# Performance work log

Measured on AMD Instinct MI355X. Metric: run time of the kernel, lower is better.

Reference implementation:

```python
import jax, jax.numpy as jnp
import numpy as np

B, D, T, H = 256, 256, 512, 512  # batch, input_dim, seq_len, hidden_dim


def setup_inputs() -> dict:
    key = jax.random.key(0)
    ks = jax.random.split(key, 7)
    s = 1.0 / np.sqrt(H)
    u = lambda k, shape: jax.random.uniform(k, shape, jnp.float32, -s, s)
    return {
        "x": jax.random.normal(ks[0], (B, D, T), jnp.float32),
        "W_ih": u(ks[1], (4 * H, D)),   # gate order: i, f, g, o (PyTorch)
        "W_hh": u(ks[2], (4 * H, H)),
        "b_ih": u(ks[3], (4 * H,)),
        "b_hh": u(ks[4], (4 * H,)),
        "W_mlp": u(ks[5], (1, H)),      # Linear(hidden_dim, num_classes=1)
        "b_mlp": u(ks[6], (1,)),
    }


def reference(x, W_ih, W_hh, b_ih, b_hh, W_mlp, b_mlp):
    # x: (B, D, T) -> (T, B, D), matching the two transposes in LSTM_model
    xs = jnp.transpose(x, (2, 0, 1))
    # Precompute input contributions for all timesteps: (T, B, 4H)
    x_gates = jnp.einsum('tbd,gd->tbg', xs, W_ih) + b_ih + b_hh
    Hh = W_hh.shape[1]

    def step(carry, xg):
        h, c = carry
        g = xg + h @ W_hh.T                      # (B, 4H)
        i = jax.nn.sigmoid(g[:, 0 * Hh:1 * Hh])
        f = jax.nn.sigmoid(g[:, 1 * Hh:2 * Hh])
        gg = jnp.tanh(g[:, 2 * Hh:3 * Hh])
        o = jax.nn.sigmoid(g[:, 3 * Hh:4 * Hh])
        c_new = f * c + i * gg
        h_new = o * jnp.tanh(c_new)
        return (h_new, c_new), h_new

    h0 = jnp.zeros((x.shape[0], Hh), x.dtype)
    c0 = jnp.zeros((x.shape[0], Hh), x.dtype)
    _, h_t = jax.lax.scan(step, (h0, c0), x_gates)   # (T, B, H)

    # MLP with num_layers=1: single Linear(H, 1) then sigmoid, per timestep.
    logits = jnp.einsum('tbh,h->tb', h_t, W_mlp[0]) + b_mlp[0]  # (T, B)
    out = jax.nn.sigmoid(logits)
    return out.T  # (B, T), matching out[..., t] layout
```

## Files before the change

kernel.cpp:

```cpp
#include <hip/hip_runtime.h>
#include <stdint.h>

#define BSZ 256
#define DIN 256
#define TLEN 512
#define HDIM 512
#define POISON 0xAAAAAAAAu

typedef _Float16 h16;
typedef unsigned int u32;
typedef unsigned long long u64;
typedef __attribute__((ext_vector_type(8))) _Float16 half8;
typedef __attribute__((ext_vector_type(4))) float f32x4;

__device__ __forceinline__ float fast_sigmoid(float x) {
    return 1.0f / (1.0f + __expf(-x));
}
__device__ __forceinline__ float fast_tanh(float x) {
    return 2.0f / (1.0f + __expf(-2.0f * x)) - 1.0f;
}

__device__ __forceinline__ u64 load_agent_u64(const u64* p) {
    return __hip_atomic_load((u64*)p, __ATOMIC_RELAXED, __HIP_MEMORY_SCOPE_AGENT);
}
__device__ __forceinline__ void store_agent_u32(u32* p, u32 v) {
    __hip_atomic_store(p, v, __ATOMIC_RELAXED, __HIP_MEMORY_SCOPE_AGENT);
}

__global__ __launch_bounds__(256)
void transpose_x(const float* __restrict__ x, h16* __restrict__ xT) {
    __shared__ h16 tl[64][72];
    const int tid = threadIdx.x;
    const int tb  = blockIdx.x & 7;
    const int bd0 = (blockIdx.x >> 3) * 64;
    const int t0  = tb * 64;
#pragma unroll
    for (int p = 0; p < 4; ++p) {
        int idx  = p * 256 + tid;
        int bd_l = idx >> 4;
        int t4   = idx & 15;
        float4 v = *(const float4*)(x + (size_t)(bd0 + bd_l) * TLEN + t0 + t4 * 4);
        tl[t4 * 4 + 0][bd_l] = (h16)v.x;
        tl[t4 * 4 + 1][bd_l] = (h16)v.y;
        tl[t4 * 4 + 2][bd_l] = (h16)v.z;
        tl[t4 * 4 + 3][bd_l] = (h16)v.w;
    }
    __syncthreads();
#pragma unroll
    for (int p = 0; p < 2; ++p) {
        int idx = p * 256 + tid;
        int t_l = idx >> 3;
        int seg = idx & 7;
        uint4 v = *(const uint4*)&tl[t_l][seg * 8];
        *(uint4*)(xT + (size_t)(t0 + t_l) * (BSZ * DIN) + bd0 + seg * 8) = v;
    }
}

__global__ __launch_bounds__(256, 1)
void lstm_kernel(const float* __restrict__ x,
                 const float* __restrict__ W_ih,
                 const float* __restrict__ W_hh,
                 const float* __restrict__ b_ih,
                 const float* __restrict__ b_hh,
                 const float* __restrict__ W_mlp,
                 const h16* __restrict__ xT,
                 int use_xT,
                 h16* __restrict__ hslots,
                 float* __restrict__ logits,
                 float* __restrict__ part,
                 int use_part)
{
    __shared__ h16  h_sw[16][64][8];
    __shared__ h16  x_sw[8][8][64][8];
    __shared__ float g_lds[16][132];

    const int tid  = threadIdx.x;
    const int bid  = blockIdx.x;
    const int clique = bid & 15;
    const int mem    = bid >> 4;
    const int lane = tid & 63;
    const int w    = tid >> 6;
    const int l15  = lane & 15;
    const int lq   = lane >> 4;
    const int cb   = clique * 16;

    half8 whh[2][16], wih[2][8];
#pragma unroll
    for (int i = 0; i < 2; ++i) {
        const int nrow = w * HDIM + mem * 32 + i * 16 + l15;
        const float* wr = W_hh + (size_t)nrow * HDIM;
#pragma unroll
        for (int kk = 0; kk < 16; ++kk) {
            const float* p = wr + kk * 32 + lq * 8;
            half8 v;
#pragma unroll
            for (int j = 0; j < 8; ++j) v[j] = (h16)p[j];
            whh[i][kk] = v;
        }
        const float* wr2 = W_ih + (size_t)nrow * DIN;
#pragma unroll
        for (int kk = 0; kk < 8; ++kk) {
            const float* p = wr2 + kk * 32 + lq * 8;
            half8 v;
#pragma unroll
            for (int j = 0; j < 8; ++j) v[j] = (h16)p[j];
            wih[i][kk] = v;
        }
    }

    const int eb = tid >> 4;
    const int ej = tid & 15;
    const int jg = mem * 32 + ej * 2;
    float bias[8];
#pragma unroll
    for (int q = 0; q < 4; ++q) {
        bias[q * 2 + 0] = b_ih[q * HDIM + jg]     + b_hh[q * HDIM + jg];
        bias[q * 2 + 1] = b_ih[q * HDIM + jg + 1] + b_hh[q * HDIM + jg + 1];
    }
    const float wm0 = W_mlp[jg], wm1 = W_mlp[jg + 1];
    float c0 = 0.0f, c1 = 0.0f;
    float pbuf[8];

    u32  qoff[8];
    h16* hdst4[4];
#pragma unroll
    for (int it = 0; it < 4; ++it) {
        int c   = it * 256 + tid;
        int L   = c & 63;
        int kk  = c >> 6;
        int b   = L & 15;
        int k0  = kk * 32 + (L >> 4) * 8;
        qoff[it * 2 + 0] = (u32)((b * HDIM + k0) >> 2);
        qoff[it * 2 + 1] = qoff[it * 2 + 0] + 1;
        hdst4[it] = &h_sw[kk][L][0];
    }
    const size_t own_off = (size_t)(cb + eb) * HDIM + jg;

    const int pfL = tid & 63;
    const int pfk = tid >> 6;
    const int pfb = pfL & 15;
    const int pfd = pfk * 32 + ((pfL >> 4) * 8);
    const h16* pf_src = xT + (size_t)(cb + pfb) * DIN + pfd;

    if (use_xT) {
        uint4 v0 = *(const uint4*)(pf_src);
        uint4 v1 = *(const uint4*)(pf_src + 128);
        *(uint4*)&x_sw[0][pfk][pfL][0]     = v0;
        *(uint4*)&x_sw[0][pfk + 4][pfL][0] = v1;
    }
    __syncthreads();

    for (int t = 0; t < TLEN; ++t) {
        if (!use_xT && (t & 7) == 0) {
            const int d   = tid;
            const int kk  = d >> 5;
            const int dlq = (d >> 3) & 3;
            const int j   = d & 7;
#pragma unroll 4
            for (int b = 0; b < 16; ++b) {
                const float* p = x + ((size_t)(cb + b) * DIN + d) * TLEN + t;
                float4 v0 = *(const float4*)p;
                float4 v1 = *(const float4*)(p + 4);
                int L = b | (dlq << 4);
                x_sw[0][kk][L][j] = (h16)v0.x;
                x_sw[1][kk][L][j] = (h16)v0.y;
                x_sw[2][kk][L][j] = (h16)v0.z;
                x_sw[3][kk][L][j] = (h16)v0.w;
                x_sw[4][kk][L][j] = (h16)v1.x;
                x_sw[5][kk][L][j] = (h16)v1.y;
                x_sw[6][kk][L][j] = (h16)v1.z;
                x_sw[7][kk][L][j] = (h16)v1.w;
            }
        }

        u64 q[8];
        u32 pend = 0;
        const u64* hb = nullptr;
        if (t > 0) {
            hb = (const u64*)(hslots + ((size_t)(t & 7) * BSZ + cb) * HDIM);
#pragma unroll
            for (int i = 0; i < 8; ++i) q[i] = load_agent_u64(hb + qoff[i]);
            asm volatile("s_waitcnt vmcnt(0)" ::: "memory");
            store_agent_u32((u32*)(hslots + (size_t)((t + 3) & 7) * BSZ * HDIM
                                          + own_off), POISON);
            u32 np = 0;
#pragma unroll
            for (int i = 0; i < 8; ++i) {
                u32 lo = (u32)q[i], hi = (u32)(q[i] >> 32);
                if (lo == POISON || hi == POISON) np |= 1u << i;
            }
            pend = np;
            if (pend) {
#pragma unroll
                for (int i = 0; i < 8; ++i)
                    if (pend & (1u << i)) q[i] = load_agent_u64(hb + qoff[i]);
            }
        }

        uint4 pf0, pf1;
        const int havepf = (use_xT && (t + 1) < TLEN);
        if (havepf) {
            const h16* ps = pf_src + (size_t)(t + 1) * (BSZ * DIN);
            pf0 = *(const uint4*)ps;
            pf1 = *(const uint4*)(ps + 128);
        }

        f32x4 acc0 = {0.f, 0.f, 0.f, 0.f};
        f32x4 acc1 = {0.f, 0.f, 0.f, 0.f};
        if (use_xT) {
            const int sx = t & 1;
#pragma unroll
            for (int kk = 0; kk < 8; ++kk) {
                half8 a = *(const half8*)&x_sw[sx][kk][lane][0];
                acc0 = __builtin_amdgcn_mfma_f32_16x16x32_f16(a, wih[0][kk], acc0, 0, 0, 0);
                acc1 = __builtin_amdgcn_mfma_f32_16x16x32_f16(a, wih[1][kk], acc1, 0, 0, 0);
            }
        }

        if (t > 0) {
            while (pend) {
                u32 np = 0;
#pragma unroll
                for (int i = 0; i < 8; ++i)
                    if (pend & (1u << i)) {
                        u32 lo = (u32)q[i], hi = (u32)(q[i] >> 32);
                        if (lo == POISON || hi == POISON) np |= 1u << i;
                    }
                pend = np;
                if (pend) {
                    __builtin_amdgcn_s_sleep(1);
#pragma unroll
                    for (int i = 0; i < 8; ++i)
                        if (pend & (1u << i)) q[i] = load_agent_u64(hb + qoff[i]);
                }
            }
#pragma unroll
            for (int it = 0; it < 4; ++it) {
                union { u64 qq[2]; uint4 v; } pk;
                pk.qq[0] = q[it * 2 + 0];
                pk.qq[1] = q[it * 2 + 1];
                *(uint4*)hdst4[it] = pk.v;
            }
        }
        __syncthreads();

        if (!use_xT) {
            const int sb = t & 7;
#pragma unroll
            for (int kk = 0; kk < 8; ++kk) {
                half8 a = *(const half8*)&x_sw[sb][kk][lane][0];
                acc0 = __builtin_amdgcn_mfma_f32_16x16x32_f16(a, wih[0][kk], acc0, 0, 0, 0);
                acc1 = __builtin_amdgcn_mfma_f32_16x16x32_f16(a, wih[1][kk], acc1, 0, 0, 0);
            }
        }
        f32x4 acc0b = {0.f, 0.f, 0.f, 0.f};
        f32x4 acc1b = {0.f, 0.f, 0.f, 0.f};
        if (t > 0) {
#pragma unroll
            for (int kk = 0; kk < 8; ++kk) {
                half8 a = *(const half8*)&h_sw[kk][lane][0];
                half8 b = *(const half8*)&h_sw[kk + 8][lane][0];
                acc0  = __builtin_amdgcn_mfma_f32_16x16x32_f16(a, whh[0][kk],     acc0,  0, 0, 0);
                acc1  = __builtin_amdgcn_mfma_f32_16x16x32_f16(a, whh[1][kk],     acc1,  0, 0, 0);
                acc0b = __builtin_amdgcn_mfma_f32_16x16x32_f16(b, whh[0][kk + 8], acc0b, 0, 0, 0);
                acc1b = __builtin_amdgcn_mfma_f32_16x16x32_f16(b, whh[1][kk + 8], acc1b, 0, 0, 0);
            }
        }
        {
            const int col0 = w * 32 + l15;
            const int col1 = w * 32 + 16 + l15;
#pragma unroll
            for (int r = 0; r < 4; ++r) {
                g_lds[lq * 4 + r][col0] = acc0[r] + acc0b[r];
                g_lds[lq * 4 + r][col1] = acc1[r] + acc1b[r];
            }
        }
        if (havepf) {
            const int sx1 = (t + 1) & 1;
            *(uint4*)&x_sw[sx1][pfk][pfL][0]     = pf0;
            *(uint4*)&x_sw[sx1][pfk + 4][pfL][0] = pf1;
        }
        __syncthreads();

        float mlp_p;
        {
            float gi0 = g_lds[eb][ej * 2]          + bias[0];
            float gi1 = g_lds[eb][ej * 2 + 1]      + bias[1];
            float gf0 = g_lds[eb][32 + ej * 2]     + bias[2];
            float gf1 = g_lds[eb][32 + ej * 2 + 1] + bias[3];
            float gg0 = g_lds[eb][64 + ej * 2]     + bias[4];
            float gg1 = g_lds[eb][64 + ej * 2 + 1] + bias[5];
            float go0 = g_lds[eb][96 + ej * 2]     + bias[6];
            float go1 = g_lds[eb][96 + ej * 2 + 1] + bias[7];
            c0 = fast_sigmoid(gf0) * c0 + fast_sigmoid(gi0) * fast_tanh(gg0);
            c1 = fast_sigmoid(gf1) * c1 + fast_sigmoid(gi1) * fast_tanh(gg1);
            float h0 = fast_sigmoid(go0) * fast_tanh(c0);
            float h1 = fast_sigmoid(go1) * fast_tanh(c1);

            union { h16 h2[2]; u32 uu; } pk;
            pk.h2[0] = (h16)h0; pk.h2[1] = (h16)h1;
            if (pk.uu == POISON) pk.uu ^= 1u;
            store_agent_u32((u32*)(hslots + (size_t)((t + 1) & 7) * BSZ * HDIM
                                          + own_off), pk.uu);

            float p = h0 * wm0 + h1 * wm1;
            p += __shfl_xor(p, 1);
            p += __shfl_xor(p, 2);
            p += __shfl_xor(p, 4);
            p += __shfl_xor(p, 8);
            mlp_p = p;
            pbuf[t & 7] = p;
            if (use_part && (t & 7) == 7 && ej == 0) {
                float* pd = &part[((size_t)mem * BSZ + cb + eb) * TLEN + (t - 7)];
                float4 v0, v1;
                v0.x = pbuf[0]; v0.y = pbuf[1]; v0.z = pbuf[2]; v0.w = pbuf[3];
                v1.x = pbuf[4]; v1.y = pbuf[5]; v1.z = pbuf[6]; v1.w = pbuf[7];
                *(float4*)pd       = v0;
                *(float4*)(pd + 4) = v1;
            }
        }
        if (!use_part && ej == 0) {
            atomicAdd(&logits[(size_t)(cb + eb) * TLEN + t], mlp_p);
        }
    }
}

__global__ __launch_bounds__(256)
void final_sigmoid(const float* __restrict__ logits,
                   const float* __restrict__ part,
                   int use_part,
                   const float* __restrict__ b_mlp,
                   float* __restrict__ out) {
    int i = blockIdx.x * 256 + threadIdx.x;
    float v;
    if (use_part) {
        int t = i & (TLEN - 1);
        int b = i >> 9;
        v = 0.f;
#pragma unroll
        for (int mm = 0; mm < 16; ++mm)
            v += part[((size_t)mm * BSZ + b) * TLEN + t];
    } else {
        v = logits[i];
    }
    v += b_mlp[0];
    out[i] = 1.0f / (1.0f + __expf(-v));
}

extern "C" void kernel_launch(void* const* d_in, const int* in_sizes, int n_in,
                              void* d_out, int out_size, void* d_ws, size_t ws_size,
                              hipStream_t stream) {
    const float* x     = (const float*)d_in[0];
    const float* W_ih  = (const float*)d_in[1];
    const float* W_hh  = (const float*)d_in[2];
    const float* b_ih  = (const float*)d_in[3];
    const float* b_hh  = (const float*)d_in[4];
    const float* W_mlp = (const float*)d_in[5];
    const float* b_mlp = (const float*)d_in[6];
    float* out = (float*)d_out;

    char* ws = (char*)d_ws;
    float* logits = (float*)ws;
    h16*   hslots = (h16*)(ws + 1048576);
    float* part   = (float*)(ws + 4194304);
    h16*   xT     = (h16*)(ws + 20971520);
    const int use_part = (ws_size >= (size_t)20971520) ? 1 : 0;
    const int use_xT   = (ws_size >= (size_t)88080384) ? 1 : 0;

    hipMemsetAsync(d_ws, 0, 524288, stream);

    if (use_xT) {
        transpose_x<<<8192, 256, 0, stream>>>(x, xT);
    }
    lstm_kernel<<<256, 256, 0, stream>>>(x, W_ih, W_hh, b_ih, b_hh, W_mlp,
                                         xT, use_xT, hslots, logits,
                                         part, use_part);
    final_sigmoid<<<(BSZ * TLEN) / 256, 256, 0, stream>>>(logits, part, use_part,
                                                          b_mlp, out);
}
```

Measured before the change: 1.857 ms.

## Remap W_hh rows per wave so gate math is wave-local, drop second barrier

Reorders the recurrent weight rows so each wave's MFMA output holds all four gates for its own 8 hidden units. The elementwise LSTM update can then read gates from a per-wave LDS tile without a block-wide barrier. The h tile is double-buffered in LDS, and the x-prefetch store and h loads are moved ahead of the single remaining barrier. MLP partial sums are now reduced per wave and stored as fp16 in 64 partial buffers, which adds precision loss and extra reads in the final reduction.

```diff
diff --git a/kernel.cpp b/kernel.cpp
--- a/kernel.cpp
+++ b/kernel.cpp
@@ -67,12 +67,12 @@
                  int use_xT,
                  h16* __restrict__ hslots,
                  float* __restrict__ logits,
-                 float* __restrict__ part,
+                 h16* __restrict__ part2,
                  int use_part)
 {
-    __shared__ h16  h_sw[16][64][8];
+    __shared__ h16  h_sw[2][16][64][8];
     __shared__ h16  x_sw[8][8][64][8];
-    __shared__ float g_lds[16][132];
+    __shared__ float gw[4][16][37];
 
     const int tid  = threadIdx.x;
     const int bid  = blockIdx.x;
@@ -87,7 +87,9 @@
     half8 whh[2][16], wih[2][8];
 #pragma unroll
     for (int i = 0; i < 2; ++i) {
-        const int nrow = w * HDIM + mem * 32 + i * 16 + l15;
+        const int gate = i * 2 + (l15 >> 3);
+        const int unit = mem * 32 + w * 8 + (l15 & 7);
+        const int nrow = gate * HDIM + unit;
         const float* wr = W_hh + (size_t)nrow * HDIM;
 #pragma unroll
         for (int kk = 0; kk < 16; ++kk) {
@@ -108,9 +110,7 @@
         }
     }
 
-    const int eb = tid >> 4;
-    const int ej = tid & 15;
-    const int jg = mem * 32 + ej * 2;
+    const int jg = mem * 32 + w * 8 + 2 * lq;
     float bias[8];
 #pragma unroll
     for (int q = 0; q < 4; ++q) {
@@ -132,9 +132,11 @@
         int k0  = kk * 32 + (L >> 4) * 8;
         qoff[it * 2 + 0] = (u32)((b * HDIM + k0) >> 2);
         qoff[it * 2 + 1] = qoff[it * 2 + 0] + 1;
-        hdst4[it] = &h_sw[kk][L][0];
-    }
-    const size_t own_off = (size_t)(cb + eb) * HDIM + jg;
+        hdst4[it] = &h_sw[0][kk][L][0];
+    }
+    const size_t own_off = (size_t)(cb + l15) * HDIM + jg;
+    const u64* hsl = (const u64*)hslots;
+    const u32 slot_u64 = (BSZ * HDIM) >> 2;
 
     const int pfL = tid & 63;
     const int pfk = tid >> 6;
@@ -151,7 +153,79 @@
     __syncthreads();
 
     for (int t = 0; t < TLEN; ++t) {
+        f32x4 acc0 = {0.f, 0.f, 0.f, 0.f};
+        f32x4 acc1 = {0.f, 0.f, 0.f, 0.f};
+        if (use_xT) {
+            const int sx = t & 1;
+#pragma unroll
+            for (int kk = 0; kk < 8; ++kk) {
+                half8 a = *(const half8*)&x_sw[sx][kk][lane][0];
+                acc0 = __builtin_amdgcn_mfma_f32_16x16x32_f16(a, wih[0][kk], acc0, 0, 0, 0);
+                acc1 = __builtin_amdgcn_mfma_f32_16x16x32_f16(a, wih[1][kk], acc1, 0, 0, 0);
+            }
+        }
+
+        u64 q[8];
+        u32 pend = 0;
+        const u64* hb = nullptr;
+        if (t > 0) {
+            hb = hsl + ((size_t)(t & 7) * BSZ + cb) * HDIM / 4;
+#pragma unroll
+            for (int i = 0; i < 8; ++i) q[i] = load_agent_u64(hb + qoff[i]);
+            asm volatile("s_waitcnt vmcnt(0)" ::: "memory");
+            store_agent_u32((u32*)(hslots + (size_t)((t + 3) & 7) * BSZ * HDIM
+                                          + own_off), POISON);
+            u32 np = 0;
+#pragma unroll
+            for (int i = 0; i < 8; ++i) {
+                u32 lo = (u32)q[i], hi = (u32)(q[i] >> 32);
+                if (lo == POISON || hi == POISON) np |= 1u << i;
+            }
+            pend = np;
+            if (pend) {
+#pragma unroll
+                for (int i = 0; i < 8; ++i)
+                    if (pend & (1u << i)) q[i] = load_agent_u64(hb + qoff[i]);
+            }
+        }
+
+        uint4 pf0, pf1;
+        const int havepf = (use_xT && (t + 1) < TLEN);
+        if (havepf) {
+            const h16* ps = pf_src + (size_t)(t + 1) * (BSZ * DIN);
+            pf0 = *(const uint4*)ps;
+            pf1 = *(const uint4*)(ps + 128);
+        }
+
+        if (t > 0) {
+            while (pend) {
+                u32 np = 0;
+#pragma unroll
+                for (int i = 0; i < 8; ++i)
+                    if (pend & (1u << i)) {
+                        u32 lo = (u32)q[i], hi = (u32)(q[i] >> 32);
+                        if (lo == POISON || hi == POISON) np |= 1u << i;
+                    }
+                pend = np;
+                if (pend) {
+                    __builtin_amdgcn_s_sleep(1);
+#pragma unroll
+                    for (int i = 0; i < 8; ++i)
+                        if (pend & (1u << i)) q[i] = load_agent_u64(hb + qoff[i]);
+                }
+            }
+            const int hoff = (t & 1) << 13;
+#pragma unroll
+            for (int it = 0; it < 4; ++it) {
+                union { u64 qq[2]; uint4 v; } pk;
+                pk.qq[0] = q[it * 2 + 0];
+                pk.qq[1] = q[it * 2 + 1];
+                *(uint4*)(hdst4[it] + hoff) = pk.v;
+            }
+        }
+
         if (!use_xT && (t & 7) == 0) {
+            __syncthreads();
             const int d   = tid;
             const int kk  = d >> 5;
             const int dlq = (d >> 3) & 3;
@@ -173,74 +247,10 @@
             }
         }
 
-        u64 q[8];
-        u32 pend = 0;
-        const u64* hb = nullptr;
-        if (t > 0) {
-            hb = (const u64*)(hslots + ((size_t)(t & 7) * BSZ + cb) * HDIM);
-#pragma unroll
-            for (int i = 0; i < 8; ++i) q[i] = load_agent_u64(hb + qoff[i]);
-            asm volatile("s_waitcnt vmcnt(0)" ::: "memory");
-            store_agent_u32((u32*)(hslots + (size_t)((t + 3) & 7) * BSZ * HDIM
-                                          + own_off), POISON);
-            u32 np = 0;
-#pragma unroll
-            for (int i = 0; i < 8; ++i) {
-                u32 lo = (u32)q[i], hi = (u32)(q[i] >> 32);
-                if (lo == POISON || hi == POISON) np |= 1u << i;
-            }
-            pend = np;
-            if (pend) {
-#pragma unroll
-                for (int i = 0; i < 8; ++i)
-                    if (pend & (1u << i)) q[i] = load_agent_u64(hb + qoff[i]);
-            }
-        }
-
-        uint4 pf0, pf1;
-        const int havepf = (use_xT && (t + 1) < TLEN);
         if (havepf) {
-            const h16* ps = pf_src + (size_t)(t + 1) * (BSZ * DIN);
-            pf0 = *(const uint4*)ps;
-            pf1 = *(const uint4*)(ps + 128);
-        }
-
-        f32x4 acc0 = {0.f, 0.f, 0.f, 0.f};
-        f32x4 acc1 = {0.f, 0.f, 0.f, 0.f};
-        if (use_xT) {
-            const int sx = t & 1;
-#pragma unroll
-            for (int kk = 0; kk < 8; ++kk) {
-                half8 a = *(const half8*)&x_sw[sx][kk][lane][0];
-                acc0 = __builtin_amdgcn_mfma_f32_16x16x32_f16(a, wih[0][kk], acc0, 0, 0, 0);
-                acc1 = __builtin_amdgcn_mfma_f32_16x16x32_f16(a, wih[1][kk], acc1, 0, 0, 0);
-            }
-        }
-
-        if (t > 0) {
-            while (pend) {
-                u32 np = 0;
-#pragma unroll
-                for (int i = 0; i < 8; ++i)
-                    if (pend & (1u << i)) {
-                        u32 lo = (u32)q[i], hi = (u32)(q[i] >> 32);
-                        if (lo == POISON || hi == POISON) np |= 1u << i;
-                    }
-                pend = np;
-                if (pend) {
-                    __builtin_amdgcn_s_sleep(1);
-#pragma unroll
-                    for (int i = 0; i < 8; ++i)
-                        if (pend & (1u << i)) q[i] = load_agent_u64(hb + qoff[i]);
-                }
-            }
-#pragma unroll
-            for (int it = 0; it < 4; ++it) {
-                union { u64 qq[2]; uint4 v; } pk;
-                pk.qq[0] = q[it * 2 + 0];
-                pk.qq[1] = q[it * 2 + 1];
-                *(uint4*)hdst4[it] = pk.v;
-            }
+            const int sx1 = (t + 1) & 1;
+            *(uint4*)&x_sw[sx1][pfk][pfL][0]     = pf0;
+            *(uint4*)&x_sw[sx1][pfk + 4][pfL][0] = pf1;
         }
         __syncthreads();
 
@@ -256,42 +266,34 @@
         f32x4 acc0b = {0.f, 0.f, 0.f, 0.f};
         f32x4 acc1b = {0.f, 0.f, 0.f, 0.f};
         if (t > 0) {
+            const h16* hbuf = &h_sw[t & 1][0][0][0];
 #pragma unroll
             for (int kk = 0; kk < 8; ++kk) {
-                half8 a = *(const half8*)&h_sw[kk][lane][0];
-                half8 b = *(const half8*)&h_sw[kk + 8][lane][0];
+                half8 a = *(const half8*)(hbuf + (kk * 64 + lane) * 8);
+                half8 b = *(const half8*)(hbuf + ((kk + 8) * 64 + lane) * 8);
                 acc0  = __builtin_amdgcn_mfma_f32_16x16x32_f16(a, whh[0][kk],     acc0,  0, 0, 0);
                 acc1  = __builtin_amdgcn_mfma_f32_16x16x32_f16(a, whh[1][kk],     acc1,  0, 0, 0);
                 acc0b = __builtin_amdgcn_mfma_f32_16x16x32_f16(b, whh[0][kk + 8], acc0b, 0, 0, 0);
                 acc1b = __builtin_amdgcn_mfma_f32_16x16x32_f16(b, whh[1][kk + 8], acc1b, 0, 0, 0);
             }
         }
+
+#pragma unroll
+        for (int r = 0; r < 4; ++r) {
+            gw[w][lq * 4 + r][l15]      = acc0[r] + acc0b[r];
+            gw[w][lq * 4 + r][16 + l15] = acc1[r] + acc1b[r];
+        }
+        asm volatile("s_waitcnt lgkmcnt(0)" ::: "memory");
+
         {
-            const int col0 = w * 32 + l15;
-            const int col1 = w * 32 + 16 + l15;
-#pragma unroll
-            for (int r = 0; r < 4; ++r) {
-                g_lds[lq * 4 + r][col0] = acc0[r] + acc0b[r];
-                g_lds[lq * 4 + r][col1] = acc1[r] + acc1b[r];
-            }
-        }
-        if (havepf) {
-            const int sx1 = (t + 1) & 1;
-            *(uint4*)&x_sw[sx1][pfk][pfL][0]     = pf0;
-            *(uint4*)&x_sw[sx1][pfk + 4][pfL][0] = pf1;
-        }
-        __syncthreads();
-
-        float mlp_p;
-        {
-            float gi0 = g_lds[eb][ej * 2]          + bias[0];
-            float gi1 = g_lds[eb][ej * 2 + 1]      + bias[1];
-            float gf0 = g_lds[eb][32 + ej * 2]     + bias[2];
-            float gf1 = g_lds[eb][32 + ej * 2 + 1] + bias[3];
-            float gg0 = g_lds[eb][64 + ej * 2]     + bias[4];
-            float gg1 = g_lds[eb][64 + ej * 2 + 1] + bias[5];
-            float go0 = g_lds[eb][96 + ej * 2]     + bias[6];
-            float go1 = g_lds[eb][96 + ej * 2 + 1] + bias[7];
+            float gi0 = gw[w][l15][2 * lq]          + bias[0];
+            float gi1 = gw[w][l15][2 * lq + 1]      + bias[1];
+            float gf0 = gw[w][l15][8 + 2 * lq]      + bias[2];
+            float gf1 = gw[w][l15][8 + 2 * lq + 1]  + bias[3];
+            float gg0 = gw[w][l15][16 + 2 * lq]     + bias[4];
+            float gg1 = gw[w][l15][16 + 2 * lq + 1] + bias[5];
+            float go0 = gw[w][l15][24 + 2 * lq]     + bias[6];
+            float go1 = gw[w][l15][24 + 2 * lq + 1] + bias[7];
             c0 = fast_sigmoid(gf0) * c0 + fast_sigmoid(gi0) * fast_tanh(gg0);
             c1 = fast_sigmoid(gf1) * c1 + fast_sigmoid(gi1) * fast_tanh(gg1);
             float h0 = fast_sigmoid(go0) * fast_tanh(c0);
@@ -304,30 +306,26 @@
                                           + own_off), pk.uu);
 
             float p = h0 * wm0 + h1 * wm1;
-            p += __shfl_xor(p, 1);
-            p += __shfl_xor(p, 2);
-            p += __shfl_xor(p, 4);
-            p += __shfl_xor(p, 8);
-            mlp_p = p;
+            p += __shfl_xor(p, 16);
+            p += __shfl_xor(p, 32);
             pbuf[t & 7] = p;
-            if (use_part && (t & 7) == 7 && ej == 0) {
-                float* pd = &part[((size_t)mem * BSZ + cb + eb) * TLEN + (t - 7)];
-                float4 v0, v1;
-                v0.x = pbuf[0]; v0.y = pbuf[1]; v0.z = pbuf[2]; v0.w = pbuf[3];
-                v1.x = pbuf[4]; v1.y = pbuf[5]; v1.z = pbuf[6]; v1.w = pbuf[7];
-                *(float4*)pd       = v0;
-                *(float4*)(pd + 4) = v1;
-            }
-        }
-        if (!use_part && ej == 0) {
-            atomicAdd(&logits[(size_t)(cb + eb) * TLEN + t], mlp_p);
+            if (use_part && (t & 7) == 7 && lq == 0) {
+                union { h16 hh[8]; uint4 v; } pp;
+#pragma unroll
+                for (int s = 0; s < 8; ++s) pp.hh[s] = (h16)pbuf[s];
+                h16* pd = part2 + ((size_t)(mem * 4 + w) * BSZ + cb + l15) * TLEN + (t - 7);
+                *(uint4*)pd = pp.v;
+            }
+            if (!use_part && lq == 0) {
+                atomicAdd(&logits[(size_t)(cb + l15) * TLEN + t], p);
+            }
         }
     }
 }
 
 __global__ __launch_bounds__(256)
 void final_sigmoid(const float* __restrict__ logits,
-                   const float* __restrict__ part,
+                   const h16* __restrict__ part2,
                    int use_part,
                    const float* __restrict__ b_mlp,
                    float* __restrict__ out) {
@@ -338,8 +336,8 @@
         int b = i >> 9;
         v = 0.f;
 #pragma unroll
-        for (int mm = 0; mm < 16; ++mm)
-            v += part[((size_t)mm * BSZ + b) * TLEN + t];
+        for (int mm = 0; mm < 64; ++mm)
+            v += (float)part2[((size_t)mm * BSZ + b) * TLEN + t];
     } else {
         v = logits[i];
     }
@@ -362,7 +360,7 @@
     char* ws = (char*)d_ws;
     float* logits = (float*)ws;
     h16*   hslots = (h16*)(ws + 1048576);
-    float* part   = (float*)(ws + 4194304);
+    h16*   part2  = (h16*)(ws + 4194304);
     h16*   xT     = (h16*)(ws + 20971520);
     const int use_part = (ws_size >= (size_t)20971520) ? 1 : 0;
     const int use_xT   = (ws_size >= (size_t)88080384) ? 1 : 0;
@@ -374,7 +372,7 @@
     }
     lstm_kernel<<<256, 256, 0, stream>>>(x, W_ih, W_hh, b_ih, b_hh, W_mlp,
                                          xT, use_xT, hslots, logits,
-                                         part, use_part);
-    final_sigmoid<<<(BSZ * TLEN) / 256, 256, 0, stream>>>(logits, part, use_part,
+                                         part2, use_part);
+    final_sigmoid<<<(BSZ * TLEN) / 256, 256, 0, stream>>>(logits, part2, use_part,
                                                           b_mlp, out);
 }
```

Measured after the change: 1.917 ms. +3.2%, slower.

## Split LSTM gate GEMM K-dimension across two wave groups per block

Applied to the files above, without the earlier changes.

Doubles the block to 512 threads and splits the K dimension of both the input and recurrent matmuls between two groups of four waves. Each group writes partial gate sums to its own LDS buffer, and the first 256 threads add the halves and run the cell update. This halves the serial MFMA chain and the h-slot loads per wave on each recurrent step, shortening the latency-bound critical path. The cost is double the register-resident weight footprint per block, an extra LDS reduction, and only half the threads doing cell work.

```diff
diff --git a/kernel.cpp b/kernel.cpp
--- a/kernel.cpp
+++ b/kernel.cpp
@@ -56,7 +56,7 @@
     }
 }
 
-__global__ __launch_bounds__(256, 1)
+__global__ __launch_bounds__(512, 1)
 void lstm_kernel(const float* __restrict__ x,
                  const float* __restrict__ W_ih,
                  const float* __restrict__ W_hh,
@@ -72,43 +72,46 @@
 {
     __shared__ h16  h_sw[16][64][8];
     __shared__ h16  x_sw[8][8][64][8];
-    __shared__ float g_lds[16][132];
+    __shared__ float g_lds[2][16][132];
 
     const int tid  = threadIdx.x;
     const int bid  = blockIdx.x;
     const int clique = bid & 15;
     const int mem    = bid >> 4;
     const int lane = tid & 63;
-    const int w    = tid >> 6;
+    const int W    = tid >> 6;
+    const int w    = W & 3;
+    const int ik   = W >> 2;
     const int l15  = lane & 15;
     const int lq   = lane >> 4;
     const int cb   = clique * 16;
-
-    half8 whh[2][16], wih[2][8];
-#pragma unroll
-    for (int i = 0; i < 2; ++i) {
-        const int nrow = w * HDIM + mem * 32 + i * 16 + l15;
-        const float* wr = W_hh + (size_t)nrow * HDIM;
-#pragma unroll
-        for (int kk = 0; kk < 16; ++kk) {
+    const int cell = (tid < 256);
+
+    half8 whh[2][8], wih[2][4];
+#pragma unroll
+    for (int j = 0; j < 2; ++j) {
+        const int nrow = w * HDIM + mem * 32 + j * 16 + l15;
+        const float* wr = W_hh + (size_t)nrow * HDIM + ik * 256;
+#pragma unroll
+        for (int kk = 0; kk < 8; ++kk) {
             const float* p = wr + kk * 32 + lq * 8;
             half8 v;
 #pragma unroll
-            for (int j = 0; j < 8; ++j) v[j] = (h16)p[j];
-            whh[i][kk] = v;
-        }
-        const float* wr2 = W_ih + (size_t)nrow * DIN;
-#pragma unroll
-        for (int kk = 0; kk < 8; ++kk) {
+            for (int jj = 0; jj < 8; ++jj) v[jj] = (h16)p[jj];
+            whh[j][kk] = v;
+        }
+        const float* wr2 = W_ih + (size_t)nrow * DIN + ik * 128;
+#pragma unroll
+        for (int kk = 0; kk < 4; ++kk) {
             const float* p = wr2 + kk * 32 + lq * 8;
             half8 v;
 #pragma unroll
-            for (int j = 0; j < 8; ++j) v[j] = (h16)p[j];
-            wih[i][kk] = v;
-        }
-    }
-
-    const int eb = tid >> 4;
+            for (int jj = 0; jj < 8; ++jj) v[jj] = (h16)p[jj];
+            wih[j][kk] = v;
+        }
+    }
+
+    const int eb = (tid >> 4) & 15;
     const int ej = tid & 15;
     const int jg = mem * 32 + ej * 2;
     float bias[8];
@@ -121,11 +124,11 @@
     float c0 = 0.0f, c1 = 0.0f;
     float pbuf[8];
 
-    u32  qoff[8];
-    h16* hdst4[4];
-#pragma unroll
-    for (int it = 0; it < 4; ++it) {
-        int c   = it * 256 + tid;
+    u32  qoff[4];
+    h16* hdst4[2];
+#pragma unroll
+    for (int it = 0; it < 2; ++it) {
+        int c   = it * 512 + tid;
         int L   = c & 63;
         int kk  = c >> 6;
         int b   = L & 15;
@@ -135,6 +138,8 @@
         hdst4[it] = &h_sw[kk][L][0];
     }
     const size_t own_off = (size_t)(cb + eb) * HDIM + jg;
+    const u64* hsl = (const u64*)hslots;
+    const u32 slot_u64 = (BSZ * HDIM) >> 2;
 
     const int pfL = tid & 63;
     const int pfk = tid >> 6;
@@ -144,14 +149,12 @@
 
     if (use_xT) {
         uint4 v0 = *(const uint4*)(pf_src);
-        uint4 v1 = *(const uint4*)(pf_src + 128);
-        *(uint4*)&x_sw[0][pfk][pfL][0]     = v0;
-        *(uint4*)&x_sw[0][pfk + 4][pfL][0] = v1;
+        *(uint4*)&x_sw[0][pfk][pfL][0] = v0;
     }
     __syncthreads();
 
     for (int t = 0; t < TLEN; ++t) {
-        if (!use_xT && (t & 7) == 0) {
+        if (!use_xT && (t & 7) == 0 && cell) {
             const int d   = tid;
             const int kk  = d >> 5;
             const int dlq = (d >> 3) & 3;
@@ -173,36 +176,36 @@
             }
         }
 
-        u64 q[8];
+        u64 q[4];
         u32 pend = 0;
         const u64* hb = nullptr;
         if (t > 0) {
-            hb = (const u64*)(hslots + ((size_t)(t & 7) * BSZ + cb) * HDIM);
-#pragma unroll
-            for (int i = 0; i < 8; ++i) q[i] = load_agent_u64(hb + qoff[i]);
+            hb = hsl + (size_t)(t & 7) * slot_u64 + ((size_t)cb * HDIM >> 2);
+#pragma unroll
+            for (int i = 0; i < 4; ++i) q[i] = load_agent_u64(hb + qoff[i]);
             asm volatile("s_waitcnt vmcnt(0)" ::: "memory");
-            store_agent_u32((u32*)(hslots + (size_t)((t + 3) & 7) * BSZ * HDIM
-                                          + own_off), POISON);
+            if (cell)
+                store_agent_u32((u32*)(hslots + (size_t)((t + 3) & 7) * BSZ * HDIM
+                                              + own_off), POISON);
             u32 np = 0;
 #pragma unroll
-            for (int i = 0; i < 8; ++i) {
+            for (int i = 0; i < 4; ++i) {
                 u32 lo = (u32)q[i], hi = (u32)(q[i] >> 32);
                 if (lo == POISON || hi == POISON) np |= 1u << i;
             }
             pend = np;
             if (pend) {
 #pragma unroll
-                for (int i = 0; i < 8; ++i)
+                for (int i = 0; i < 4; ++i)
                     if (pend & (1u << i)) q[i] = load_agent_u64(hb + qoff[i]);
             }
         }
 
-        uint4 pf0, pf1;
+        uint4 pf0;
         const int havepf = (use_xT && (t + 1) < TLEN);
         if (havepf) {
             const h16* ps = pf_src + (size_t)(t + 1) * (BSZ * DIN);
             pf0 = *(const uint4*)ps;
-            pf1 = *(const uint4*)(ps + 128);
         }
 
         f32x4 acc0 = {0.f, 0.f, 0.f, 0.f};
@@ -210,8 +213,8 @@
         if (use_xT) {
             const int sx = t & 1;
 #pragma unroll
-            for (int kk = 0; kk < 8; ++kk) {
-                half8 a = *(const half8*)&x_sw[sx][kk][lane][0];
+            for (int kk = 0; kk < 4; ++kk) {
+                half8 a = *(const half8*)&x_sw[sx][ik * 4 + kk][lane][0];
                 acc0 = __builtin_amdgcn_mfma_f32_16x16x32_f16(a, wih[0][kk], acc0, 0, 0, 0);
                 acc1 = __builtin_amdgcn_mfma_f32_16x16x32_f16(a, wih[1][kk], acc1, 0, 0, 0);
             }
@@ -221,7 +224,7 @@
             while (pend) {
                 u32 np = 0;
 #pragma unroll
-                for (int i = 0; i < 8; ++i)
+                for (int i = 0; i < 4; ++i)
                     if (pend & (1u << i)) {
                         u32 lo = (u32)q[i], hi = (u32)(q[i] >> 32);
                         if (lo == POISON || hi == POISON) np |= 1u << i;
@@ -230,12 +233,12 @@
                 if (pend) {
                     __builtin_amdgcn_s_sleep(1);
 #pragma unroll
-                    for (int i = 0; i < 8; ++i)
+                    for (int i = 0; i < 4; ++i)
                         if (pend & (1u << i)) q[i] = load_agent_u64(hb + qoff[i]);
                 }
             }
 #pragma unroll
-            for (int it = 0; it < 4; ++it) {
+            for (int it = 0; it < 2; ++it) {
                 union { u64 qq[2]; uint4 v; } pk;
                 pk.qq[0] = q[it * 2 + 0];
                 pk.qq[1] = q[it * 2 + 1];
@@ -247,23 +250,18 @@
         if (!use_xT) {
             const int sb = t & 7;
 #pragma unroll
-            for (int kk = 0; kk < 8; ++kk) {
-                half8 a = *(const half8*)&x_sw[sb][kk][lane][0];
+            for (int kk = 0; kk < 4; ++kk) {
+                half8 a = *(const half8*)&x_sw[sb][ik * 4 + kk][lane][0];
                 acc0 = __builtin_amdgcn_mfma_f32_16x16x32_f16(a, wih[0][kk], acc0, 0, 0, 0);
                 acc1 = __builtin_amdgcn_mfma_f32_16x16x32_f16(a, wih[1][kk], acc1, 0, 0, 0);
             }
         }
-        f32x4 acc0b = {0.f, 0.f, 0.f, 0.f};
-        f32x4 acc1b = {0.f, 0.f, 0.f, 0.f};
         if (t > 0) {
 #pragma unroll
             for (int kk = 0; kk < 8; ++kk) {
-                half8 a = *(const half8*)&h_sw[kk][lane][0];
-                half8 b = *(const half8*)&h_sw[kk + 8][lane][0];
-                acc0  = __builtin_amdgcn_mfma_f32_16x16x32_f16(a, whh[0][kk],     acc0,  0, 0, 0);
-                acc1  = __builtin_amdgcn_mfma_f32_16x16x32_f16(a, whh[1][kk],     acc1,  0, 0, 0);
-                acc0b = __builtin_amdgcn_mfma_f32_16x16x32_f16(b, whh[0][kk + 8], acc0b, 0, 0, 0);
-                acc1b = __builtin_amdgcn_mfma_f32_16x16x32_f16(b, whh[1][kk + 8], acc1b, 0, 0, 0);
+                half8 a = *(const half8*)&h_sw[ik * 8 + kk][lane][0];
+                acc0 = __builtin_amdgcn_mfma_f32_16x16x32_f16(a, whh[0][kk], acc0, 0, 0, 0);
+                acc1 = __builtin_amdgcn_mfma_f32_16x16x32_f16(a, whh[1][kk], acc1, 0, 0, 0);
             }
         }
         {
@@ -271,27 +269,24 @@
             const int col1 = w * 32 + 16 + l15;
 #pragma unroll
             for (int r = 0; r < 4; ++r) {
-                g_lds[lq * 4 + r][col0] = acc0[r] + acc0b[r];
-                g_lds[lq * 4 + r][col1] = acc1[r] + acc1b[r];
+                g_lds[ik][lq * 4 + r][col0] = acc0[r];
+                g_lds[ik][lq * 4 + r][col1] = acc1[r];
             }
         }
         if (havepf) {
-            const int sx1 = (t + 1) & 1;
-            *(uint4*)&x_sw[sx1][pfk][pfL][0]     = pf0;
-            *(uint4*)&x_sw[sx1][pfk + 4][pfL][0] = pf1;
+            *(uint4*)&x_sw[(t + 1) & 1][pfk][pfL][0] = pf0;
         }
         __syncthreads();
 
-        float mlp_p;
-        {
-            float gi0 = g_lds[eb][ej * 2]          + bias[0];
-            float gi1 = g_lds[eb][ej * 2 + 1]      + bias[1];
-            float gf0 = g_lds[eb][32 + ej * 2]     + bias[2];
-            float gf1 = g_lds[eb][32 + ej * 2 + 1] + bias[3];
-            float gg0 = g_lds[eb][64 + ej * 2]     + bias[4];
-            float gg1 = g_lds[eb][64 + ej * 2 + 1] + bias[5];
-            float go0 = g_lds[eb][96 + ej * 2]     + bias[6];
-            float go1 = g_lds[eb][96 + ej * 2 + 1] + bias[7];
+        if (cell) {
+            float gi0 = g_lds[0][eb][ej * 2]          + g_lds[1][eb][ej * 2]          + bias[0];
+            float gi1 = g_lds[0][eb][ej * 2 + 1]      + g_lds[1][eb][ej * 2 + 1]      + bias[1];
+            float gf0 = g_lds[0][eb][32 + ej * 2]     + g_lds[1][eb][32 + ej * 2]     + bias[2];
+            float gf1 = g_lds[0][eb][32 + ej * 2 + 1] + g_lds[1][eb][32 + ej * 2 + 1] + bias[3];
+            float gg0 = g_lds[0][eb][64 + ej * 2]     + g_lds[1][eb][64 + ej * 2]     + bias[4];
+            float gg1 = g_lds[0][eb][64 + ej * 2 + 1] + g_lds[1][eb][64 + ej * 2 + 1] + bias[5];
+            float go0 = g_lds[0][eb][96 + ej * 2]     + g_lds[1][eb][96 + ej * 2]     + bias[6];
+            float go1 = g_lds[0][eb][96 + ej * 2 + 1] + g_lds[1][eb][96 + ej * 2 + 1] + bias[7];
             c0 = fast_sigmoid(gf0) * c0 + fast_sigmoid(gi0) * fast_tanh(gg0);
             c1 = fast_sigmoid(gf1) * c1 + fast_sigmoid(gi1) * fast_tanh(gg1);
             float h0 = fast_sigmoid(go0) * fast_tanh(c0);
@@ -308,7 +303,6 @@
             p += __shfl_xor(p, 2);
             p += __shfl_xor(p, 4);
             p += __shfl_xor(p, 8);
-            mlp_p = p;
             pbuf[t & 7] = p;
             if (use_part && (t & 7) == 7 && ej == 0) {
                 float* pd = &part[((size_t)mem * BSZ + cb + eb) * TLEN + (t - 7)];
@@ -318,9 +312,9 @@
                 *(float4*)pd       = v0;
                 *(float4*)(pd + 4) = v1;
             }
-        }
-        if (!use_part && ej == 0) {
-            atomicAdd(&logits[(size_t)(cb + eb) * TLEN + t], mlp_p);
+            if (!use_part && ej == 0) {
+                atomicAdd(&logits[(size_t)(cb + eb) * TLEN + t], p);
+            }
         }
     }
 }
@@ -372,7 +366,7 @@
     if (use_xT) {
         transpose_x<<<8192, 256, 0, stream>>>(x, xT);
     }
-    lstm_kernel<<<256, 256, 0, stream>>>(x, W_ih, W_hh, b_ih, b_hh, W_mlp,
+    lstm_kernel<<<256, 512, 0, stream>>>(x, W_ih, W_hh, b_ih, b_hh, W_mlp,
                                          xT, use_xT, hslots, logits,
                                          part, use_part);
     final_sigmoid<<<(BSZ * TLEN) / 256, 256, 0, stream>>>(logits, part, use_part,
```

New measurement: 2.503 ms. 34.8% more time.

## Split batch into 32 cliques of 8 rows, two LSTM blocks per CU

Applied to the files above, without the earlier changes.

The recurrent kernel now runs 512 blocks in 32 cliques of 8 batch rows each, instead of 16 cliques of 16 rows, with launch bounds allowing two blocks per CU. Per-step hidden-state gathers and x prefetches are halved per block, and only the first 128 threads do the cell update. The goal is to interleave two independent recurrences per CU so each hides the other's cross-block synchronisation latency. In exchange the MFMA tiles stay 16 rows wide with half the rows unused, so per-CU matrix work doubles. Correctness also now depends on all 512 spinning blocks being resident at once.

```diff
diff --git a/kernel.cpp b/kernel.cpp
--- a/kernel.cpp
+++ b/kernel.cpp
@@ -6,6 +6,8 @@
 #define TLEN 512
 #define HDIM 512
 #define POISON 0xAAAAAAAAu
+#define NCLQ 32
+#define CB   8
 
 typedef _Float16 h16;
 typedef unsigned int u32;
@@ -56,7 +58,7 @@
     }
 }
 
-__global__ __launch_bounds__(256, 1)
+__global__ __launch_bounds__(256, 2)
 void lstm_kernel(const float* __restrict__ x,
                  const float* __restrict__ W_ih,
                  const float* __restrict__ W_hh,
@@ -71,18 +73,19 @@
                  int use_part)
 {
     __shared__ h16  h_sw[16][64][8];
-    __shared__ h16  x_sw[8][8][64][8];
+    __shared__ h16  x_sw[2][8][64][8];
     __shared__ float g_lds[16][132];
 
     const int tid  = threadIdx.x;
     const int bid  = blockIdx.x;
-    const int clique = bid & 15;
-    const int mem    = bid >> 4;
+    const int clique = bid & (NCLQ - 1);
+    const int mem    = bid >> 5;
     const int lane = tid & 63;
     const int w    = tid >> 6;
     const int l15  = lane & 15;
     const int lq   = lane >> 4;
-    const int cb   = clique * 16;
+    const int cb   = clique * CB;
+    const int cell = (tid < 16 * CB);
 
     half8 whh[2][16], wih[2][8];
 #pragma unroll
@@ -108,7 +111,7 @@
         }
     }
 
-    const int eb = tid >> 4;
+    const int eb = (tid >> 4) & 15;
     const int ej = tid & 15;
     const int jg = mem * 32 + ej * 2;
     float bias[8];
@@ -121,88 +124,76 @@
     float c0 = 0.0f, c1 = 0.0f;
     float pbuf[8];
 
-    u32  qoff[8];
-    h16* hdst4[4];
-#pragma unroll
-    for (int it = 0; it < 4; ++it) {
+    u32  qoff[4];
+    h16* hdst4[2];
+#pragma unroll
+    for (int it = 0; it < 2; ++it) {
         int c   = it * 256 + tid;
-        int L   = c & 63;
-        int kk  = c >> 6;
-        int b   = L & 15;
-        int k0  = kk * 32 + (L >> 4) * 8;
-        qoff[it * 2 + 0] = (u32)((b * HDIM + k0) >> 2);
+        int b   = c & 7;
+        int lqs = (c >> 3) & 3;
+        int kk  = c >> 5;
+        int el  = b * HDIM + kk * 32 + lqs * 8;
+        qoff[it * 2 + 0] = (u32)(el >> 2);
         qoff[it * 2 + 1] = qoff[it * 2 + 0] + 1;
-        hdst4[it] = &h_sw[kk][L][0];
+        hdst4[it] = &h_sw[kk][lqs * 16 + b][0];
     }
     const size_t own_off = (size_t)(cb + eb) * HDIM + jg;
-
-    const int pfL = tid & 63;
-    const int pfk = tid >> 6;
-    const int pfb = pfL & 15;
-    const int pfd = pfk * 32 + ((pfL >> 4) * 8);
-    const h16* pf_src = xT + (size_t)(cb + pfb) * DIN + pfd;
+    const u64* hsl = (const u64*)hslots;
+    const u32 slot_u64 = (BSZ * HDIM) >> 2;
+    const u64* hb_base = hsl + ((size_t)cb * HDIM >> 2);
+
+    const int pfb = tid & 7;
+    const int pflq = (tid >> 3) & 3;
+    const int pfk = tid >> 5;
+    const h16* pf_src = xT + (size_t)(cb + pfb) * DIN + pfk * 32 + pflq * 8;
+    h16* const pf_dst0 = &x_sw[0][pfk][pflq * 16 + pfb][0];
+    h16* const pf_dst1 = &x_sw[1][pfk][pflq * 16 + pfb][0];
 
     if (use_xT) {
-        uint4 v0 = *(const uint4*)(pf_src);
-        uint4 v1 = *(const uint4*)(pf_src + 128);
-        *(uint4*)&x_sw[0][pfk][pfL][0]     = v0;
-        *(uint4*)&x_sw[0][pfk + 4][pfL][0] = v1;
+        *(uint4*)pf_dst0 = *(const uint4*)(pf_src);
     }
     __syncthreads();
 
     for (int t = 0; t < TLEN; ++t) {
-        if (!use_xT && (t & 7) == 0) {
-            const int d   = tid;
-            const int kk  = d >> 5;
-            const int dlq = (d >> 3) & 3;
-            const int j   = d & 7;
-#pragma unroll 4
-            for (int b = 0; b < 16; ++b) {
-                const float* p = x + ((size_t)(cb + b) * DIN + d) * TLEN + t;
-                float4 v0 = *(const float4*)p;
-                float4 v1 = *(const float4*)(p + 4);
-                int L = b | (dlq << 4);
-                x_sw[0][kk][L][j] = (h16)v0.x;
-                x_sw[1][kk][L][j] = (h16)v0.y;
-                x_sw[2][kk][L][j] = (h16)v0.z;
-                x_sw[3][kk][L][j] = (h16)v0.w;
-                x_sw[4][kk][L][j] = (h16)v1.x;
-                x_sw[5][kk][L][j] = (h16)v1.y;
-                x_sw[6][kk][L][j] = (h16)v1.z;
-                x_sw[7][kk][L][j] = (h16)v1.w;
-            }
-        }
-
-        u64 q[8];
+        if (!use_xT) {
+            const int b  = tid >> 5;
+            const int d0 = (tid & 31) * 8;
+            for (int j = 0; j < 8; ++j) {
+                int d = d0 + j;
+                float v = x[((size_t)(cb + b) * DIN + d) * TLEN + t];
+                x_sw[t & 1][d >> 5][((d >> 3) & 3) * 16 + b][d & 7] = (h16)v;
+            }
+        }
+
+        u64 q[4];
         u32 pend = 0;
         const u64* hb = nullptr;
         if (t > 0) {
-            hb = (const u64*)(hslots + ((size_t)(t & 7) * BSZ + cb) * HDIM);
-#pragma unroll
-            for (int i = 0; i < 8; ++i) q[i] = load_agent_u64(hb + qoff[i]);
+            hb = hb_base + (size_t)(t & 7) * slot_u64;
+#pragma unroll
+            for (int i = 0; i < 4; ++i) q[i] = load_agent_u64(hb + qoff[i]);
             asm volatile("s_waitcnt vmcnt(0)" ::: "memory");
-            store_agent_u32((u32*)(hslots + (size_t)((t + 3) & 7) * BSZ * HDIM
-                                          + own_off), POISON);
+            if (cell)
+                store_agent_u32((u32*)(hslots + (size_t)((t + 3) & 7) * BSZ * HDIM
+                                              + own_off), POISON);
             u32 np = 0;
 #pragma unroll
-            for (int i = 0; i < 8; ++i) {
+            for (int i = 0; i < 4; ++i) {
                 u32 lo = (u32)q[i], hi = (u32)(q[i] >> 32);
                 if (lo == POISON || hi == POISON) np |= 1u << i;
             }
             pend = np;
             if (pend) {
 #pragma unroll
-                for (int i = 0; i < 8; ++i)
+                for (int i = 0; i < 4; ++i)
                     if (pend & (1u << i)) q[i] = load_agent_u64(hb + qoff[i]);
             }
         }
 
-        uint4 pf0, pf1;
+        uint4 pf0;
         const int havepf = (use_xT && (t + 1) < TLEN);
         if (havepf) {
-            const h16* ps = pf_src + (size_t)(t + 1) * (BSZ * DIN);
-            pf0 = *(const uint4*)ps;
-            pf1 = *(const uint4*)(ps + 128);
+            pf0 = *(const uint4*)(pf_src + (size_t)(t + 1) * (BSZ * DIN));
         }
 
         f32x4 acc0 = {0.f, 0.f, 0.f, 0.f};
@@ -221,7 +212,7 @@
             while (pend) {
                 u32 np = 0;
 #pragma unroll
-                for (int i = 0; i < 8; ++i)
+                for (int i = 0; i < 4; ++i)
                     if (pend & (1u << i)) {
                         u32 lo = (u32)q[i], hi = (u32)(q[i] >> 32);
                         if (lo == POISON || hi == POISON) np |= 1u << i;
@@ -230,12 +221,12 @@
                 if (pend) {
                     __builtin_amdgcn_s_sleep(1);
 #pragma unroll
-                    for (int i = 0; i < 8; ++i)
+                    for (int i = 0; i < 4; ++i)
                         if (pend & (1u << i)) q[i] = load_agent_u64(hb + qoff[i]);
                 }
             }
 #pragma unroll
-            for (int it = 0; it < 4; ++it) {
+            for (int it = 0; it < 2; ++it) {
                 union { u64 qq[2]; uint4 v; } pk;
                 pk.qq[0] = q[it * 2 + 0];
                 pk.qq[1] = q[it * 2 + 1];
@@ -245,7 +236,7 @@
         __syncthreads();
 
         if (!use_xT) {
-            const int sb = t & 7;
+            const int sb = t & 1;
 #pragma unroll
             for (int kk = 0; kk < 8; ++kk) {
                 half8 a = *(const half8*)&x_sw[sb][kk][lane][0];
@@ -276,14 +267,11 @@
             }
         }
         if (havepf) {
-            const int sx1 = (t + 1) & 1;
-            *(uint4*)&x_sw[sx1][pfk][pfL][0]     = pf0;
-            *(uint4*)&x_sw[sx1][pfk + 4][pfL][0] = pf1;
+            *(uint4*)(((t + 1) & 1) ? pf_dst1 : pf_dst0) = pf0;
         }
         __syncthreads();
 
-        float mlp_p;
-        {
+        if (cell) {
             float gi0 = g_lds[eb][ej * 2]          + bias[0];
             float gi1 = g_lds[eb][ej * 2 + 1]      + bias[1];
             float gf0 = g_lds[eb][32 + ej * 2]     + bias[2];
@@ -308,7 +296,6 @@
             p += __shfl_xor(p, 2);
             p += __shfl_xor(p, 4);
             p += __shfl_xor(p, 8);
-            mlp_p = p;
             pbuf[t & 7] = p;
             if (use_part && (t & 7) == 7 && ej == 0) {
                 float* pd = &part[((size_t)mem * BSZ + cb + eb) * TLEN + (t - 7)];
@@ -318,9 +305,9 @@
                 *(float4*)pd       = v0;
                 *(float4*)(pd + 4) = v1;
             }
-        }
-        if (!use_part && ej == 0) {
-            atomicAdd(&logits[(size_t)(cb + eb) * TLEN + t], mlp_p);
+            if (!use_part && ej == 0) {
+                atomicAdd(&logits[(size_t)(cb + eb) * TLEN + t], p);
+            }
         }
     }
 }
@@ -372,7 +359,7 @@
     if (use_xT) {
         transpose_x<<<8192, 256, 0, stream>>>(x, xT);
     }
-    lstm_kernel<<<256, 256, 0, stream>>>(x, W_ih, W_hh, b_ih, b_hh, W_mlp,
+    lstm_kernel<<<512, 256, 0, stream>>>(x, W_ih, W_hh, b_ih, b_hh, W_mlp,
                                          xT, use_xT, hslots, logits,
                                          part, use_part);
     final_sigmoid<<<(BSZ * TLEN) / 256, 256, 0, stream>>>(logits, part, use_part,
```

After: 3.624 ms. +95.2%, slower.
